# Kernel tuning notes

Measured on AMD Instinct MI355X. Metric: run time of the kernel, lower is better.

The kernel has to match this reference:

```python
import jax, jax.numpy as jnp
import numpy as np

SEG_LENS = (2048, 4096, 8192)
DIL_RATES = (1, 2, 4)
NUM_HEADS = 12
HEAD_DIM = 64
LN_EPS = 1e-5


def _dilated_attention(q, k, v):
    # q,k,v: [b, n, h, d]; heads partitioned across (segment, dilation) groups
    b, n, h, d = q.shape
    G = len(SEG_LENS)
    hg = h // G
    scale = d ** -0.5
    out = jnp.zeros_like(q)
    for i, (s, r) in enumerate(zip(SEG_LENS, DIL_RATES)):
        hmin = i * hg
        m = n // s                      # number of segments
        idx = jnp.arange(i % r, s, r)   # dilated positions within a segment, len = s // r
        def seg(t):
            # [b, n, hg, d] -> [b, m, s//r, hg, d]
            return t[:, :, hmin:hmin + hg, :].reshape(b, m, s, hg, d)[:, :, idx]
        qs, ks, vs = seg(q), seg(k), seg(v)
        scores = jnp.einsum('bmshd,bmthd->bmhst', qs, ks) * scale  # [b,m,hg,s/r,s/r]
        attn = jax.nn.softmax(scores, axis=-1)
        o = jnp.einsum('bmhst,bmthd->bmshd', attn, vs)              # [b,m,s/r,hg,d]
        pos = (jnp.arange(m)[:, None] * s + idx[None, :]).reshape(-1)
        out = out.at[:, pos, hmin:hmin + hg, :].set(o.reshape(b, -1, hg, d))
    return out


def setup_inputs() -> dict:
    key = jax.random.key(0)
    ks = jax.random.split(key, 4)
    E = NUM_HEADS * HEAD_DIM
    b, n = 1, 8192
    x = jax.random.normal(ks[0], (b, n, E), dtype=jnp.float32)
    w_qkv = jax.random.normal(ks[1], (3 * E, E), dtype=jnp.float32) * (E ** -0.5)
    b_qkv = jnp.zeros((3 * E,), dtype=jnp.float32)
    w_out = jax.random.normal(ks[2], (E, E), dtype=jnp.float32) * (E ** -0.5)
    b_out = jnp.zeros((E,), dtype=jnp.float32)
    ln_gamma = jnp.ones((E,), dtype=jnp.float32)
    ln_beta = jnp.zeros((E,), dtype=jnp.float32)
    return {'x': x, 'w_qkv': w_qkv, 'b_qkv': b_qkv, 'w_out': w_out,
            'b_out': b_out, 'ln_gamma': ln_gamma, 'ln_beta': ln_beta}


def reference(x, w_qkv, b_qkv, w_out, b_out, ln_gamma, ln_beta):
    b, n, E = x.shape
    qkv = x @ w_qkv.T + b_qkv
    q, k, v = jnp.split(qkv, 3, axis=-1)
    shp = (b, n, NUM_HEADS, HEAD_DIM)
    o = _dilated_attention(q.reshape(shp), k.reshape(shp), v.reshape(shp)).reshape(b, n, E)
    # MAGNETO: LayerNorm on attention output before out projection
    mu = jnp.mean(o, axis=-1, keepdims=True)
    var = jnp.mean(jnp.square(o - mu), axis=-1, keepdims=True)
    on = (o - mu) / jnp.sqrt(var + LN_EPS) * ln_gamma + ln_beta
    return on @ w_out.T + b_out
```

## Files before the change

kernel.cpp:

```cpp
#include <hip/hip_runtime.h>
#include <hip/hip_bf16.h>
#include <cstdint>
#include <cstddef>


typedef __attribute__((ext_vector_type(8))) short short8;
typedef __attribute__((ext_vector_type(4))) short short4_;
typedef __attribute__((ext_vector_type(4))) float float4_;

__device__ __forceinline__ float bf2f(short s) {
    unsigned int u = ((unsigned int)(unsigned short)s) << 16;
    float f;
    __builtin_memcpy(&f, &u, 4);
    return f;
}
__device__ __forceinline__ short f2bf(float f) {
    unsigned int u;
    __builtin_memcpy(&u, &f, 4);
    u += 0x7fffu + ((u >> 16) & 1u);
    return (short)(u >> 16);
}
__device__ __forceinline__ short f2bf_trunc(float f) {
    unsigned int u;
    __builtin_memcpy(&u, &f, 4);
    return (short)(u >> 16);
}
__device__ __forceinline__ short8 f8_to_bf8(const float* __restrict__ p) {
    float4_ a = *(const float4_*)(p);
    float4_ b = *(const float4_*)(p + 4);
    short8 r;
    r[0] = f2bf(a[0]); r[1] = f2bf(a[1]); r[2] = f2bf(a[2]); r[3] = f2bf(a[3]);
    r[4] = f2bf(b[0]); r[5] = f2bf(b[1]); r[6] = f2bf(b[2]); r[7] = f2bf(b[3]);
    return r;
}
__device__ __forceinline__ void gll16(const short* g, short* l) {
    __builtin_amdgcn_global_load_lds(
        (const __attribute__((address_space(1))) unsigned int*)g,
        (__attribute__((address_space(3))) unsigned int*)l, 16, 0, 0);
}

#define LDT 72

__global__ __launch_bounds__(256) void cvt3(
    const float* __restrict__ a, int na, const float* __restrict__ b, int nb,
    const float* __restrict__ c, int nc,
    short* __restrict__ oa, short* __restrict__ ob, short* __restrict__ oc)
{
    int i = (blockIdx.x * 256 + threadIdx.x) * 8;
    if (i < na) {
        *(short8*)&oa[i] = f8_to_bf8(a + i);
    } else if (i < na + nb) {
        int j = i - na;
        *(short8*)&ob[j] = f8_to_bf8(b + j);
    } else {
        int j = i - na - nb;
        if (j < nc) *(short8*)&oc[j] = f8_to_bf8(c + j);
    }
}

template<int EPI>
__global__ __launch_bounds__(256) void gemm128(
    const short* __restrict__ A, int lda,
    const short* __restrict__ B,
    const float* __restrict__ bias,
    void* __restrict__ Cv,
    int N, int K)
{
    __shared__ short As[128 * 64];
    __shared__ short Bs[128 * 64];
    const int tid  = threadIdx.x;
    const int wave = tid >> 6, lane = tid & 63;
    const int quad = lane >> 4, l16 = lane & 15;
    const int wr = wave >> 1, wc = wave & 1;
    const int m0 = blockIdx.y * 128, n0 = blockIdx.x * 128;
    const int lrow   = lane >> 3;
    const int lchunk = (lane & 7) ^ lrow;

    const short* Abase = A + (size_t)(m0 + wave * 32 + lrow) * lda + lchunk * 8;
    const short* Bbase = B + (size_t)(n0 + wave * 32 + lrow) * (size_t)K + lchunk * 8;
    short* AsW = &As[(wave * 32) * 64];
    short* BsW = &Bs[(wave * 32) * 64];

    float4_ acc[4][4] = {};

    for (int k0 = 0; k0 < K; k0 += 64) {
        __syncthreads();
        #pragma unroll
        for (int i = 0; i < 4; i++) {
            gll16(Abase + (size_t)(i * 8) * lda + k0, AsW + (i * 8) * 64);
            gll16(Bbase + (size_t)(i * 8) * K   + k0, BsW + (i * 8) * 64);
        }
        __syncthreads();
        #pragma unroll
        for (int ks = 0; ks < 2; ks++) {
            short8 af[4], bf[4];
            const int ca = ((ks * 4 + quad) ^ (l16 & 7)) * 8;
            #pragma unroll
            for (int t = 0; t < 4; t++) {
                af[t] = *(const short8*)&As[(wr * 64 + t * 16 + l16) * 64 + ca];
                bf[t] = *(const short8*)&Bs[(wc * 64 + t * 16 + l16) * 64 + ca];
            }
            #pragma unroll
            for (int mt = 0; mt < 4; mt++)
                #pragma unroll
                for (int nt = 0; nt < 4; nt++)
                    acc[mt][nt] = __builtin_amdgcn_mfma_f32_16x16x32_bf16(
                        af[mt], bf[nt], acc[mt][nt], 0, 0, 0);
        }
    }

    #pragma unroll
    for (int nt = 0; nt < 4; nt++) {
        const int col = n0 + wc * 64 + nt * 16 + l16;
        const float bv = bias[col];
        if constexpr (EPI == 0) {
            short* C = (short*)Cv;
            const int g = col >> 8;
            #pragma unroll
            for (int mt = 0; mt < 4; mt++) {
                #pragma unroll
                for (int r = 0; r < 4; r++) {
                    int row = m0 + wr * 64 + mt * 16 + quad * 4 + r;
                    bool cov = (col >= 768) || (g == 0) ||
                               (g == 1 && (row & 1) == 1) ||
                               (g == 2 && (row & 3) == 2);
                    C[(size_t)row * N + col] = cov ? f2bf(acc[mt][nt][r] + bv) : (short)0;
                }
            }
        } else {
            float* C = (float*)Cv;
            #pragma unroll
            for (int mt = 0; mt < 4; mt++)
                #pragma unroll
                for (int r = 0; r < 4; r++) {
                    int row = m0 + wr * 64 + mt * 16 + quad * 4 + r;
                    C[(size_t)row * N + col] = acc[mt][nt][r] + bv;
                }
        }
    }
}

__global__ __launch_bounds__(256, 4) void dilated_attn_split(
    const short* __restrict__ qkv, short* __restrict__ Obuf,
    float* __restrict__ lbuf)
{
    __shared__ short Ks[64 * 64];
    __shared__ short Vt[64 * LDT];
    __shared__ short Ps[4 * 32 * LDT];

    const int bx = blockIdx.x;
    const int h  = bx & 1;
    const int qt = (bx >> 1) & 15;
    const int sh = bx >> 5;

    int g, seg, s, rate, off0;
    if (sh < 16)      { g = 0; seg = sh >> 2;        s = 2048; rate = 1; off0 = 0; }
    else if (sh < 24) { g = 1; seg = (sh - 16) >> 2; s = 4096; rate = 2; off0 = 1; }
    else              { g = 2; seg = 0;              s = 8192; rate = 4; off0 = 2; }
    const int head = g * 4 + (sh & 3);

    const int tid  = threadIdx.x;
    const int wave = tid >> 6, lane = tid & 63, quad = lane >> 4, l16 = lane & 15;
    const int srow = tid >> 2, scol = (tid & 3) * 16;

    short8 aq[2][2];
    #pragma unroll
    for (int rg = 0; rg < 2; rg++) {
        int t = qt * 128 + wave * 32 + rg * 16 + l16;
        size_t pos = (size_t)seg * s + off0 + (size_t)t * rate;
        const short* qsrc = qkv + pos * 2304 + head * 64 + quad * 8;
        #pragma unroll
        for (int ks = 0; ks < 2; ks++) {
            short8 q = *(const short8*)(qsrc + ks * 32);
            #pragma unroll
            for (int e = 0; e < 8; e++) q[e] = f2bf(bf2f(q[e]) * 0.125f);
            aq[rg][ks] = q;
        }
    }

    const int krow0  = wave * 8 + (lane >> 3);
    const int kchunk = (lane & 7) ^ (lane >> 3);
    const size_t kstep = (size_t)64 * rate * 2304;
    int k0 = h * 16 * 64;
    const short* kg0 = qkv + ((size_t)seg * s + off0 + (size_t)(k0 + krow0) * rate) * 2304
                           + 768 + head * 64 + kchunk * 8;
    const short* kg1 = kg0 + (size_t)32 * rate * 2304;
    short* kd0 = &Ks[(wave * 8) * 64];
    short* kd1 = kd0 + 32 * 64;
    const short* vg = qkv + ((size_t)seg * s + off0 + (size_t)(k0 + srow) * rate) * 2304
                          + 1536 + head * 64 + scol;

    float lrow[2][4] = {};
    float4_ oacc[2][4] = {};
    short* pw = &Ps[wave * 32 * LDT];
    const int cswap = (lane >> 5) & 1;
    const int pswz  = (l16 & 8) << 1;
    const int vswz  = scol;

    for (int j = 0; j < 16; j++) {
        __syncthreads();
        gll16(kg0, kd0);
        gll16(kg1, kd1);
        {
            short8 v0 = *(const short8*)(vg);
            short8 v1 = *(const short8*)(vg + 8);
            #pragma unroll
            for (int e = 0; e < 8; e++) Vt[(scol + e) * LDT + (srow ^ vswz)] = v0[e];
            #pragma unroll
            for (int e = 0; e < 8; e++) Vt[(scol + 8 + e) * LDT + (srow ^ vswz)] = v1[e];
        }
        kg0 += kstep; kg1 += kstep; vg += kstep;
        __syncthreads();

        float4_ sacc[2][4] = {};
        #pragma unroll
        for (int ks = 0; ks < 2; ks++) {
            #pragma unroll
            for (int kt = 0; kt < 4; kt++) {
                short8 bk = *(const short8*)&Ks[(kt * 16 + l16) * 64
                                                + (((quad + 4 * ks) ^ (l16 & 7)) * 8)];
                #pragma unroll
                for (int rg = 0; rg < 2; rg++)
                    sacc[rg][kt] = __builtin_amdgcn_mfma_f32_16x16x32_bf16(
                        aq[rg][ks], bk, sacc[rg][kt], 0, 0, 0);
            }
        }

        #pragma unroll
        for (int rg = 0; rg < 2; rg++) {
            #pragma unroll
            for (int r = 0; r < 4; r++) {
                float p0 = __expf(sacc[rg][0][r]), p1 = __expf(sacc[rg][1][r]);
                float p2 = __expf(sacc[rg][2][r]), p3 = __expf(sacc[rg][3][r]);
                short* prow = &pw[(rg * 16 + quad * 4 + r) * LDT + l16];
                prow[(0 ^ cswap) * 16] = f2bf_trunc(p0);
                prow[(1 ^ cswap) * 16] = f2bf_trunc(p1);
                prow[(2 ^ cswap) * 16] = f2bf_trunc(p2);
                prow[(3 ^ cswap) * 16] = f2bf_trunc(p3);
                lrow[rg][r] += (p0 + p1) + (p2 + p3);
            }
        }

        #pragma unroll
        for (int ks = 0; ks < 2; ks++) {
            short8 ap[2];
            #pragma unroll
            for (int rg = 0; rg < 2; rg++)
                ap[rg] = *(const short8*)&pw[(rg * 16 + l16) * LDT
                                             + ((ks * 32 + quad * 8) ^ pswz)];
            #pragma unroll
            for (int nt = 0; nt < 4; nt++) {
                short8 bv = *(const short8*)&Vt[(nt * 16 + l16) * LDT
                                                + ((ks * 32 + quad * 8) ^ (nt * 16))];
                #pragma unroll
                for (int rg = 0; rg < 2; rg++)
                    oacc[rg][nt] = __builtin_amdgcn_mfma_f32_16x16x32_bf16(
                        ap[rg], bv, oacc[rg][nt], 0, 0, 0);
            }
        }
    }

    #pragma unroll
    for (int rg = 0; rg < 2; rg++) {
        #pragma unroll
        for (int r = 0; r < 4; r++) {
            float v = lrow[rg][r];
            #pragma unroll
            for (int off = 1; off < 16; off <<= 1) v += __shfl_xor(v, off, 64);
            int qrow = wave * 32 + rg * 16 + quad * 4 + r;
            short* od = Obuf + ((size_t)bx * 128 + qrow) * 64;
            #pragma unroll
            for (int nt = 0; nt < 4; nt++)
                od[nt * 16 + l16] = f2bf(oacc[rg][nt][r]);
            if (l16 == 0) lbuf[(size_t)bx * 128 + qrow] = v;
        }
    }
}

__global__ __launch_bounds__(256) void attn_combine(
    const short* __restrict__ Obuf, const float* __restrict__ lbuf,
    short* __restrict__ qkv)
{
    const int p  = blockIdx.x;
    const int qt = p & 15;
    const int sh = p >> 4;

    int g, seg, s, rate, off0;
    if (sh < 16)      { g = 0; seg = sh >> 2;        s = 2048; rate = 1; off0 = 0; }
    else if (sh < 24) { g = 1; seg = (sh - 16) >> 2; s = 4096; rate = 2; off0 = 1; }
    else              { g = 2; seg = 0;              s = 8192; rate = 4; off0 = 2; }
    const int head = g * 4 + (sh & 3);

    const int tid = threadIdx.x;
    const int row = tid >> 1, dbase = (tid & 1) * 32;

    const short* o0 = Obuf + ((size_t)(p * 2) * 128 + row) * 64 + dbase;
    const short* o1 = o0 + 128 * 64;
    const float  li = 1.0f / (lbuf[(size_t)(p * 2) * 128 + row] +
                              lbuf[(size_t)(p * 2 + 1) * 128 + row]);

    int t = qt * 128 + row;
    size_t pos = (size_t)seg * s + off0 + (size_t)t * rate;
    short* dst = qkv + pos * 2304 + head * 64 + dbase;

    #pragma unroll
    for (int c = 0; c < 4; c++) {
        short8 a = *(const short8*)(o0 + c * 8);
        short8 b = *(const short8*)(o1 + c * 8);
        short8 r;
        #pragma unroll
        for (int e = 0; e < 8; e++) r[e] = f2bf((bf2f(a[e]) + bf2f(b[e])) * li);
        *(short8*)(dst + c * 8) = r;
    }
}

__global__ __launch_bounds__(256) void ln_inplace(
    short* __restrict__ qkv, const float* __restrict__ gamma,
    const float* __restrict__ beta)
{
    const int row  = blockIdx.x * 4 + (threadIdx.x >> 6);
    const int lane = threadIdx.x & 63;
    short* src = qkv + (size_t)row * 2304;

    short8  a = *(const short8*)&src[lane * 8];
    short4_ b = *(const short4_*)&src[512 + lane * 4];
    float v[12];
    #pragma unroll
    for (int e = 0; e < 8; e++) v[e] = bf2f(a[e]);
    #pragma unroll
    for (int e = 0; e < 4; e++) v[8 + e] = bf2f(b[e]);

    float sum = 0.f, sq = 0.f;
    #pragma unroll
    for (int e = 0; e < 12; e++) { sum += v[e]; sq += v[e] * v[e]; }
    #pragma unroll
    for (int off = 1; off < 64; off <<= 1) {
        sum += __shfl_xor(sum, off, 64);
        sq  += __shfl_xor(sq,  off, 64);
    }
    float mean = sum * (1.0f / 768.0f);
    float var  = sq * (1.0f / 768.0f) - mean * mean;
    float rstd = rsqrtf(var + 1e-5f);

    short8 o8; short4_ o4;
    #pragma unroll
    for (int e = 0; e < 8; e++)
        o8[e] = f2bf((v[e] - mean) * rstd * gamma[lane * 8 + e] + beta[lane * 8 + e]);
    #pragma unroll
    for (int e = 0; e < 4; e++)
        o4[e] = f2bf((v[8 + e] - mean) * rstd * gamma[512 + lane * 4 + e] + beta[512 + lane * 4 + e]);

    *(short8*)&src[lane * 8] = o8;
    *(short4_*)&src[512 + lane * 4] = o4;
}

extern "C" void kernel_launch(void* const* d_in, const int* in_sizes, int n_in,
                              void* d_out, int out_size, void* d_ws, size_t ws_size,
                              hipStream_t stream) {
    const float* x     = (const float*)d_in[0];
    const float* w_qkv = (const float*)d_in[1];
    const float* b_qkv = (const float*)d_in[2];
    const float* w_out = (const float*)d_in[3];
    const float* b_out = (const float*)d_in[4];
    const float* gamma = (const float*)d_in[5];
    const float* beta  = (const float*)d_in[6];
    float* out = (float*)d_out;

    const int NX = 8192 * 768, NW1 = 2304 * 768, NW2 = 768 * 768;
    char* ws = (char*)d_ws;
    short* qkv   = (short*)(ws);
    short* xb    = (short*)(ws + (size_t)8192 * 2304 * 2);
    short* wqkvb = xb + NX;
    short* woutb = wqkvb + NW1;
    float* lbuf  = (float*)(woutb + NW2);
    short* Obuf  = xb;

    cvt3<<<dim3((NX + NW1 + NW2) / (256 * 8)), 256, 0, stream>>>(
        x, NX, w_qkv, NW1, w_out, NW2, xb, wqkvb, woutb);

    gemm128<0><<<dim3(2304 / 128, 8192 / 128), 256, 0, stream>>>(
        xb, 768, wqkvb, b_qkv, qkv, 2304, 768);

    dilated_attn_split<<<dim3(28 * 16 * 2), 256, 0, stream>>>(qkv, Obuf, lbuf);

    attn_combine<<<dim3(28 * 16), 256, 0, stream>>>(Obuf, lbuf, qkv);

    ln_inplace<<<dim3(8192 / 4), 256, 0, stream>>>(qkv, gamma, beta);

    gemm128<1><<<dim3(768 / 128, 8192 / 128), 256, 0, stream>>>(
        qkv, 2304, woutb, b_out, out, 768, 768);
}
```

Baseline: 220.3 us.

## Drop split-K attention, fold normalization into LayerNorm, double-buffer K/V, use exp2

The attention kernel now processes the full key range per block (448 blocks, 32 iterations) instead of two key halves, which removes the separate combine kernel and the intermediate O buffer round trip. The unnormalized output is written directly into the qkv buffer, and per-row reciprocal sums go to an lbuf indexed by position and head. The LayerNorm kernel applies those reciprocals before computing statistics. K/V tiles are double-buffered in LDS with V prefetched into registers, so each iteration needs one barrier instead of two. The softmax uses a hardware exp2 with log2(e) folded into the Q scale. In exchange, half as many blocks are launched and occupancy drops to 3, and lbuf entries for positions a head group does not cover are never written, so uninitialized values get multiplied by zero.

```diff
diff --git a/kernel.cpp b/kernel.cpp
--- a/kernel.cpp
+++ b/kernel.cpp
@@ -7,6 +7,12 @@
 typedef __attribute__((ext_vector_type(8))) short short8;
 typedef __attribute__((ext_vector_type(4))) short short4_;
 typedef __attribute__((ext_vector_type(4))) float float4_;
+
+#if __has_builtin(__builtin_amdgcn_exp2f)
+#define EXP2(x) __builtin_amdgcn_exp2f(x)
+#else
+#define EXP2(x) exp2f(x)
+#endif
 
 __device__ __forceinline__ float bf2f(short s) {
     unsigned int u = ((unsigned int)(unsigned short)s) << 16;
@@ -140,18 +146,16 @@
     }
 }
 
-__global__ __launch_bounds__(256, 4) void dilated_attn_split(
-    const short* __restrict__ qkv, short* __restrict__ Obuf,
-    float* __restrict__ lbuf)
+__global__ __launch_bounds__(256, 3) void dilated_attn(
+    short* __restrict__ qkv, float* __restrict__ lbuf)
 {
-    __shared__ short Ks[64 * 64];
-    __shared__ short Vt[64 * LDT];
+    __shared__ short Ks[2 * 64 * 64];
+    __shared__ short Vt[2 * 64 * LDT];
     __shared__ short Ps[4 * 32 * LDT];
 
     const int bx = blockIdx.x;
-    const int h  = bx & 1;
-    const int qt = (bx >> 1) & 15;
-    const int sh = bx >> 5;
+    const int qt = bx & 15;
+    const int sh = bx >> 4;
 
     int g, seg, s, rate, off0;
     if (sh < 16)      { g = 0; seg = sh >> 2;        s = 2048; rate = 1; off0 = 0; }
@@ -173,7 +177,7 @@
         for (int ks = 0; ks < 2; ks++) {
             short8 q = *(const short8*)(qsrc + ks * 32);
             #pragma unroll
-            for (int e = 0; e < 8; e++) q[e] = f2bf(bf2f(q[e]) * 0.125f);
+            for (int e = 0; e < 8; e++) q[e] = f2bf(bf2f(q[e]) * 0.1803368801111244f);
             aq[rg][ks] = q;
         }
     }
@@ -181,43 +185,62 @@
     const int krow0  = wave * 8 + (lane >> 3);
     const int kchunk = (lane & 7) ^ (lane >> 3);
     const size_t kstep = (size_t)64 * rate * 2304;
-    int k0 = h * 16 * 64;
-    const short* kg0 = qkv + ((size_t)seg * s + off0 + (size_t)(k0 + krow0) * rate) * 2304
+    const short* kg0 = qkv + ((size_t)seg * s + off0 + (size_t)krow0 * rate) * 2304
                            + 768 + head * 64 + kchunk * 8;
     const short* kg1 = kg0 + (size_t)32 * rate * 2304;
-    short* kd0 = &Ks[(wave * 8) * 64];
-    short* kd1 = kd0 + 32 * 64;
-    const short* vg = qkv + ((size_t)seg * s + off0 + (size_t)(k0 + srow) * rate) * 2304
-                          + 1536 + head * 64 + scol;
+    const short* vgp = qkv + ((size_t)seg * s + off0 + (size_t)srow * rate) * 2304
+                           + 1536 + head * 64 + scol;
+    const int kofsA = (wave * 8) * 64;
+    const int kofsB = kofsA + 32 * 64;
+    const int vswz  = scol;
+
+    gll16(kg0, &Ks[kofsA]);
+    gll16(kg1, &Ks[kofsB]);
+    kg0 += kstep; kg1 += kstep;
+    short8 va0 = *(const short8*)(vgp);
+    short8 va1 = *(const short8*)(vgp + 8);
+    vgp += kstep;
+    #pragma unroll
+    for (int e = 0; e < 8; e++) Vt[(scol + e) * LDT + (srow ^ vswz)] = va0[e];
+    #pragma unroll
+    for (int e = 0; e < 8; e++) Vt[(scol + 8 + e) * LDT + (srow ^ vswz)] = va1[e];
+    va0 = *(const short8*)(vgp);
+    va1 = *(const short8*)(vgp + 8);
+    vgp += kstep;
 
     float lrow[2][4] = {};
     float4_ oacc[2][4] = {};
     short* pw = &Ps[wave * 32 * LDT];
     const int cswap = (lane >> 5) & 1;
     const int pswz  = (l16 & 8) << 1;
-    const int vswz  = scol;
-
-    for (int j = 0; j < 16; j++) {
+
+    for (int j = 0; j < 32; j++) {
         __syncthreads();
-        gll16(kg0, kd0);
-        gll16(kg1, kd1);
-        {
-            short8 v0 = *(const short8*)(vg);
-            short8 v1 = *(const short8*)(vg + 8);
-            #pragma unroll
-            for (int e = 0; e < 8; e++) Vt[(scol + e) * LDT + (srow ^ vswz)] = v0[e];
-            #pragma unroll
-            for (int e = 0; e < 8; e++) Vt[(scol + 8 + e) * LDT + (srow ^ vswz)] = v1[e];
-        }
-        kg0 += kstep; kg1 += kstep; vg += kstep;
-        __syncthreads();
+        if (j < 31) {
+            const int nb = (j + 1) & 1;
+            gll16(kg0, &Ks[nb * 4096 + kofsA]);
+            gll16(kg1, &Ks[nb * 4096 + kofsB]);
+            kg0 += kstep; kg1 += kstep;
+            short* vt = &Vt[nb * 64 * LDT];
+            #pragma unroll
+            for (int e = 0; e < 8; e++) vt[(scol + e) * LDT + (srow ^ vswz)] = va0[e];
+            #pragma unroll
+            for (int e = 0; e < 8; e++) vt[(scol + 8 + e) * LDT + (srow ^ vswz)] = va1[e];
+            if (j < 30) {
+                va0 = *(const short8*)(vgp);
+                va1 = *(const short8*)(vgp + 8);
+                vgp += kstep;
+            }
+        }
+        const short* kb = &Ks[(j & 1) * 4096];
+        const short* vb = &Vt[(j & 1) * 64 * LDT];
 
         float4_ sacc[2][4] = {};
         #pragma unroll
         for (int ks = 0; ks < 2; ks++) {
             #pragma unroll
             for (int kt = 0; kt < 4; kt++) {
-                short8 bk = *(const short8*)&Ks[(kt * 16 + l16) * 64
+                short8 bk = *(const short8*)&kb[(kt * 16 + l16) * 64
                                                 + (((quad + 4 * ks) ^ (l16 & 7)) * 8)];
                 #pragma unroll
                 for (int rg = 0; rg < 2; rg++)
@@ -230,8 +253,8 @@
         for (int rg = 0; rg < 2; rg++) {
             #pragma unroll
             for (int r = 0; r < 4; r++) {
-                float p0 = __expf(sacc[rg][0][r]), p1 = __expf(sacc[rg][1][r]);
-                float p2 = __expf(sacc[rg][2][r]), p3 = __expf(sacc[rg][3][r]);
+                float p0 = EXP2(sacc[rg][0][r]), p1 = EXP2(sacc[rg][1][r]);
+                float p2 = EXP2(sacc[rg][2][r]), p3 = EXP2(sacc[rg][3][r]);
                 short* prow = &pw[(rg * 16 + quad * 4 + r) * LDT + l16];
                 prow[(0 ^ cswap) * 16] = f2bf_trunc(p0);
                 prow[(1 ^ cswap) * 16] = f2bf_trunc(p1);
@@ -250,7 +273,7 @@
                                              + ((ks * 32 + quad * 8) ^ pswz)];
             #pragma unroll
             for (int nt = 0; nt < 4; nt++) {
-                short8 bv = *(const short8*)&Vt[(nt * 16 + l16) * LDT
+                short8 bv = *(const short8*)&vb[(nt * 16 + l16) * LDT
                                                 + ((ks * 32 + quad * 8) ^ (nt * 16))];
                 #pragma unroll
                 for (int rg = 0; rg < 2; rg++)
@@ -268,67 +291,35 @@
             #pragma unroll
             for (int off = 1; off < 16; off <<= 1) v += __shfl_xor(v, off, 64);
             int qrow = wave * 32 + rg * 16 + quad * 4 + r;
-            short* od = Obuf + ((size_t)bx * 128 + qrow) * 64;
+            int t = qt * 128 + qrow;
+            size_t pos = (size_t)seg * s + off0 + (size_t)t * rate;
+            short* od = qkv + pos * 2304 + head * 64;
             #pragma unroll
             for (int nt = 0; nt < 4; nt++)
                 od[nt * 16 + l16] = f2bf(oacc[rg][nt][r]);
-            if (l16 == 0) lbuf[(size_t)bx * 128 + qrow] = v;
-        }
-    }
-}
-
-__global__ __launch_bounds__(256) void attn_combine(
-    const short* __restrict__ Obuf, const float* __restrict__ lbuf,
-    short* __restrict__ qkv)
-{
-    const int p  = blockIdx.x;
-    const int qt = p & 15;
-    const int sh = p >> 4;
-
-    int g, seg, s, rate, off0;
-    if (sh < 16)      { g = 0; seg = sh >> 2;        s = 2048; rate = 1; off0 = 0; }
-    else if (sh < 24) { g = 1; seg = (sh - 16) >> 2; s = 4096; rate = 2; off0 = 1; }
-    else              { g = 2; seg = 0;              s = 8192; rate = 4; off0 = 2; }
-    const int head = g * 4 + (sh & 3);
-
-    const int tid = threadIdx.x;
-    const int row = tid >> 1, dbase = (tid & 1) * 32;
-
-    const short* o0 = Obuf + ((size_t)(p * 2) * 128 + row) * 64 + dbase;
-    const short* o1 = o0 + 128 * 64;
-    const float  li = 1.0f / (lbuf[(size_t)(p * 2) * 128 + row] +
-                              lbuf[(size_t)(p * 2 + 1) * 128 + row]);
-
-    int t = qt * 128 + row;
-    size_t pos = (size_t)seg * s + off0 + (size_t)t * rate;
-    short* dst = qkv + pos * 2304 + head * 64 + dbase;
-
-    #pragma unroll
-    for (int c = 0; c < 4; c++) {
-        short8 a = *(const short8*)(o0 + c * 8);
-        short8 b = *(const short8*)(o1 + c * 8);
-        short8 r;
-        #pragma unroll
-        for (int e = 0; e < 8; e++) r[e] = f2bf((bf2f(a[e]) + bf2f(b[e])) * li);
-        *(short8*)(dst + c * 8) = r;
+            if (l16 == 0) lbuf[pos * 12 + head] = 1.0f / v;
+        }
     }
 }
 
 __global__ __launch_bounds__(256) void ln_inplace(
-    short* __restrict__ qkv, const float* __restrict__ gamma,
-    const float* __restrict__ beta)
+    short* __restrict__ qkv, const float* __restrict__ lbuf,
+    const float* __restrict__ gamma, const float* __restrict__ beta)
 {
     const int row  = blockIdx.x * 4 + (threadIdx.x >> 6);
     const int lane = threadIdx.x & 63;
     short* src = qkv + (size_t)row * 2304;
 
+    const float li1 = lbuf[row * 12 + (lane >> 3)];
+    const float li2 = lbuf[row * 12 + 8 + (lane >> 4)];
+
     short8  a = *(const short8*)&src[lane * 8];
     short4_ b = *(const short4_*)&src[512 + lane * 4];
     float v[12];
     #pragma unroll
-    for (int e = 0; e < 8; e++) v[e] = bf2f(a[e]);
-    #pragma unroll
-    for (int e = 0; e < 4; e++) v[8 + e] = bf2f(b[e]);
+    for (int e = 0; e < 8; e++) v[e] = bf2f(a[e]) * li1;
+    #pragma unroll
+    for (int e = 0; e < 4; e++) v[8 + e] = bf2f(b[e]) * li2;
 
     float sum = 0.f, sq = 0.f;
     #pragma unroll
@@ -373,7 +364,6 @@
     short* wqkvb = xb + NX;
     short* woutb = wqkvb + NW1;
     float* lbuf  = (float*)(woutb + NW2);
-    short* Obuf  = xb;
 
     cvt3<<<dim3((NX + NW1 + NW2) / (256 * 8)), 256, 0, stream>>>(
         x, NX, w_qkv, NW1, w_out, NW2, xb, wqkvb, woutb);
@@ -381,11 +371,9 @@
     gemm128<0><<<dim3(2304 / 128, 8192 / 128), 256, 0, stream>>>(
         xb, 768, wqkvb, b_qkv, qkv, 2304, 768);
 
-    dilated_attn_split<<<dim3(28 * 16 * 2), 256, 0, stream>>>(qkv, Obuf, lbuf);
-
-    attn_combine<<<dim3(28 * 16), 256, 0, stream>>>(Obuf, lbuf, qkv);
-
-    ln_inplace<<<dim3(8192 / 4), 256, 0, stream>>>(qkv, gamma, beta);
+    dilated_attn<<<dim3(28 * 16), 256, 0, stream>>>(qkv, lbuf);
+
+    ln_inplace<<<dim3(8192 / 4), 256, 0, stream>>>(qkv, lbuf, gamma, beta);
 
     gemm128<1><<<dim3(768 / 128, 8192 / 128), 256, 0, stream>>>(
         qkv, 2304, woutb, b_out, out, 768, 768);
```

New measurement: 217.3 us. No clear change (-1.3%).
